# Optimization experiments

Measured on AMD Instinct MI355X. Metric: run time of the kernel, lower is better.

The kernel has to match this reference:

```python
import jax, jax.numpy as jnp
import numpy as np

# Dimensions (see shape_source)
L = 1024   # episode_len (memory slots)
B = 64     # batch (parallel envs)
K = 512    # key_size
V = 512    # value_size
H = 8      # num_head
MEMB = 256 # memory_state_embedding
SDIM = 512 # state_dim
HID = 512  # hidden width of all 2-layer encoders
RIMQ = 512 # rim_query_size
LAT = K - MEMB  # task_inference_latent dim


def setup_inputs() -> dict:
    key = jax.random.key(0)
    ks = jax.random.split(key, 16)
    w = lambda k, shape: (jax.random.normal(k, shape, jnp.float32) * 0.02)
    return {
        "state": jax.random.normal(ks[0], (B, SDIM), jnp.float32),
        "task_inference_latent": jax.random.normal(ks[1], (B, LAT), jnp.float32),
        "keys": jax.random.normal(ks[2], (L, B, K), jnp.float32),
        "vals": jax.random.normal(ks[3], (L, B, V), jnp.float32),
        "rpe_mod": jax.random.uniform(ks[4], (L, B, 1), jnp.float32),
        "step": jnp.maximum(jax.random.randint(ks[5], (B,), 0, L), 1),
        "W_state": w(ks[6], (SDIM, MEMB)), "b_state": jnp.zeros((MEMB,), jnp.float32),
        "Wcq1": w(ks[7], (K, HID)), "bcq1": jnp.zeros((HID,), jnp.float32),
        "Wcq2": w(ks[8], (HID, K)), "bcq2": jnp.zeros((K,), jnp.float32),
        "Wq": w(ks[9], (K, H * K)), "bq": jnp.zeros((H * K,), jnp.float32),
        "Wagg": w(ks[10], (H * V, V)), "bagg": jnp.zeros((V,), jnp.float32),
        "Wrk1": w(ks[11], (V, HID)), "brk1": jnp.zeros((HID,), jnp.float32),
        "Wrk2": w(ks[12], (HID, RIMQ)), "brk2": jnp.zeros((RIMQ,), jnp.float32),
        "Wrv1": w(ks[13], (V, HID)), "brv1": jnp.zeros((HID,), jnp.float32),
        "Wrv2": w(ks[14], (HID, V)), "brv2": jnp.zeros((V,), jnp.float32),
    }


def reference(state, task_inference_latent, keys, vals, rpe_mod, step,
              W_state, b_state, Wcq1, bcq1, Wcq2, bcq2, Wq, bq, Wagg, bagg,
              Wrk1, brk1, Wrk2, brk2, Wrv1, brv1, Wrv2, brv2):
    # DND.read (exploration branch), vectorized over the batch loop.
    se = state @ W_state + b_state                         # state_encoder: [B, MEMB]
    q = jnp.concatenate([se, task_inference_latent], -1)   # [B, K]
    # concat_query_encoder: stacked Linears with NO nonlinearity (faithful to source)
    q = (q @ Wcq1 + bcq1) @ Wcq2 + bcq2                    # [B, K]
    q = (q @ Wq + bq).reshape(B, H, K)                     # multi-head queries

    mk = keys * rpe_mod                                    # RPE-modulated keys [L, B, K]
    scores = jnp.einsum('lbk,bhk->blh', mk, q) / jnp.sqrt(jnp.float32(K))  # [B, L, H]
    valid = jnp.arange(L)[None, :] < step[:, None]         # [B, L] only slots < step[i]
    scores = jnp.where(valid[:, :, None], scores, jnp.float32(-1e30))
    prob = jax.nn.softmax(scores, axis=1) * valid[:, :, None].astype(scores.dtype)

    result = jnp.einsum('blh,lbv->bhv', prob, vals).reshape(B, H * V)
    result = (result @ Wagg + bagg)[:, None, :]            # value_aggregator -> [B, 1, V]
    out_key = (result @ Wrk1 + brk1) @ Wrk2 + brk2         # read_memory_to_key  [B, 1, RIMQ]
    out_val = (result @ Wrv1 + brv1) @ Wrv2 + brv2         # read_memory_to_value [B, 1, V]
    return out_key, out_val
```

## Files before the change

kernel.cpp:

```cpp
#include <hip/hip_runtime.h>
#include <math.h>

#define F4(p)  (*reinterpret_cast<float4*>(p))
#define CF4(p) (*reinterpret_cast<const float4*>(p))

__device__ __forceinline__ void gemm_core(
    const float* __restrict__ Asrc, const float* __restrict__ inbias,
    const float* __restrict__ til,
    int NS, int srcld, int kc, int k0,
    const float* __restrict__ W, int ldw, int n0,
    const float* __restrict__ obias, float* __restrict__ Pout, int ldo)
{
    __shared__ float As[16*64], Ws[16*64];
    const int t = threadIdx.x;
    const int tx = t & 15, ty = t >> 4;
    const int row = t >> 2, kq = (t & 3) * 4;
    const int wrow = t >> 4, wcol = (t & 15) * 4;
    float acc[4][4] = {};
    for (int kk = 0; kk < kc; kk += 16) {
        const int kg = k0 + kk + kq;
        float4 av;
        if (til && kg >= 256) {
            av = CF4(&til[row*256 + (kg - 256)]);
        } else {
            av = {0.f, 0.f, 0.f, 0.f};
            if (inbias) av = CF4(&inbias[kg]);
            for (int s = 0; s < NS; ++s) {
                float4 v = CF4(&Asrc[(size_t)(s*64 + row)*srcld + kg]);
                av.x += v.x; av.y += v.y; av.z += v.z; av.w += v.w;
            }
        }
        As[(kq+0)*64+row] = av.x; As[(kq+1)*64+row] = av.y;
        As[(kq+2)*64+row] = av.z; As[(kq+3)*64+row] = av.w;
        F4(&Ws[wrow*64 + wcol]) = CF4(&W[(size_t)(k0 + kk + wrow)*ldw + n0 + wcol]);
        __syncthreads();
        #pragma unroll
        for (int k = 0; k < 16; ++k) {
            float4 a4 = CF4(&As[k*64 + ty*4]);
            float4 w4 = CF4(&Ws[k*64 + tx*4]);
            float a[4] = {a4.x, a4.y, a4.z, a4.w};
            float w[4] = {w4.x, w4.y, w4.z, w4.w};
            #pragma unroll
            for (int i = 0; i < 4; ++i)
                #pragma unroll
                for (int j = 0; j < 4; ++j)
                    acc[i][j] += a[i] * w[j];
        }
        __syncthreads();
    }
    #pragma unroll
    for (int i = 0; i < 4; ++i) {
        float4 o = {acc[i][0], acc[i][1], acc[i][2], acc[i][3]};
        if (obias) {
            float4 ob = CF4(&obias[n0 + tx*4]);
            o.x += ob.x; o.y += ob.y; o.z += ob.z; o.w += ob.w;
        }
        F4(&Pout[(size_t)(ty*4 + i)*ldo + n0 + tx*4]) = o;
    }
}

__global__ __launch_bounds__(256) void k_q1(
    const float* __restrict__ state, const float* __restrict__ W_state,
    float* __restrict__ P1)
{
    const int nt = blockIdx.x, ks = blockIdx.y;
    gemm_core(state, nullptr, nullptr, 1, 512, 64, ks*64,
              W_state, 256, nt*64, nullptr, P1 + (size_t)ks*64*256, 256);
}

__global__ __launch_bounds__(256) void k_q2(
    const float* __restrict__ P1, const float* __restrict__ b_state,
    const float* __restrict__ til, const float* __restrict__ Wcq1,
    float* __restrict__ P2)
{
    const int nt = blockIdx.x, ks = blockIdx.y;
    gemm_core(P1, b_state, til, 8, 256, 64, ks*64,
              Wcq1, 512, nt*64, nullptr, P2 + (size_t)ks*64*512, 512);
}

__global__ __launch_bounds__(256) void k_q3(
    const float* __restrict__ P2, const float* __restrict__ bcq1,
    const float* __restrict__ Wcq2, float* __restrict__ P3)
{
    const int nt = blockIdx.x, ks = blockIdx.y;
    gemm_core(P2, bcq1, nullptr, 8, 512, 64, ks*64,
              Wcq2, 512, nt*64, nullptr, P3 + (size_t)ks*64*512, 512);
}

__global__ __launch_bounds__(256) void k_qh(
    const float* __restrict__ P3, const float* __restrict__ bcq2,
    const float* __restrict__ Wq, float* __restrict__ P4)
{
    const int nt = blockIdx.x, ks = blockIdx.y;
    gemm_core(P3, bcq2, nullptr, 8, 512, 128, ks*128,
              Wq, 4096, nt*64, nullptr, P4 + (size_t)ks*64*4096, 4096);
}

__global__ __launch_bounds__(256) void k_fa(
    const float* __restrict__ keys, const float* __restrict__ rpe,
    const float* __restrict__ P4, const float* __restrict__ bq,
    const float* __restrict__ vals, const int* __restrict__ step,
    float* __restrict__ Facc, float* __restrict__ Fms)
{
    __shared__ float s_q[4096];
    __shared__ float s_sc[64*8];
    __shared__ float red[256];
    __shared__ float s_m[8];
    const int b = blockIdx.y, lc = blockIdx.x;
    const int sb = step[b];
    const int l0 = lc * 64;
    const int t = threadIdx.x;
    float* facc_out = Facc + ((size_t)(lc*64) + b)*4096;
    if (l0 >= sb) {
        float4 z = {0.f, 0.f, 0.f, 0.f};
        for (int i = t; i < 1024; i += 256) F4(&facc_out[i*4]) = z;
        if (t < 8) {
            size_t o = ((size_t)(lc*64 + b)*8 + t)*2;
            Fms[o] = -1e30f; Fms[o+1] = 0.f;
        }
        return;
    }
    for (int i = t; i < 1024; i += 256) {
        float4 v = CF4(&bq[i*4]);
        #pragma unroll
        for (int s = 0; s < 4; ++s) {
            float4 u = CF4(&P4[(size_t)(s*64 + b)*4096 + i*4]);
            v.x += u.x; v.y += u.y; v.z += u.z; v.w += u.w;
        }
        F4(&s_q[i*4]) = v;
    }
    __syncthreads();
    const int lane = t & 63, w = t >> 6;
    float qr[8][8];
    #pragma unroll
    for (int h = 0; h < 8; ++h) {
        float4 x = CF4(&s_q[h*512 + lane*8]);
        float4 y = CF4(&s_q[h*512 + lane*8 + 4]);
        qr[h][0]=x.x; qr[h][1]=x.y; qr[h][2]=x.z; qr[h][3]=x.w;
        qr[h][4]=y.x; qr[h][5]=y.y; qr[h][6]=y.z; qr[h][7]=y.w;
    }
    const int nl = min(64, sb - l0);
    const float inv_sqrtK = 0.04419417382415922f;
    const bool p0 = lane & 1, p1 = lane & 2, p2 = lane & 4;
    const size_t kstride = (size_t)4*64*512;
    const float* kp = keys + ((size_t)(l0 + w)*64 + b)*512 + lane*8;
    float4 kx, ky;
    if (w < nl) { kx = CF4(kp); ky = CF4(kp + 4); }
    for (int il = w; il < nl; il += 4) {
        float4 nkx, nky;
        if (il + 4 < nl) { nkx = CF4(kp + kstride); nky = CF4(kp + kstride + 4); }
        float kv[8] = {kx.x,kx.y,kx.z,kx.w, ky.x,ky.y,ky.z,ky.w};
        float pr[8] = {};
        #pragma unroll
        for (int h = 0; h < 8; ++h)
            #pragma unroll
            for (int j = 0; j < 8; ++j)
                pr[h] += kv[j] * qr[h][j];
        float w4[4], x2[2], y;
        #pragma unroll
        for (int i = 0; i < 4; ++i) {
            float keep = p0 ? pr[2*i+1] : pr[2*i];
            float send = p0 ? pr[2*i]   : pr[2*i+1];
            w4[i] = keep + __shfl_xor(send, 1);
        }
        #pragma unroll
        for (int i = 0; i < 2; ++i) {
            float keep = p1 ? w4[2*i+1] : w4[2*i];
            float send = p1 ? w4[2*i]   : w4[2*i+1];
            x2[i] = keep + __shfl_xor(send, 2);
        }
        {
            float keep = p2 ? x2[1] : x2[0];
            float send = p2 ? x2[0] : x2[1];
            y = keep + __shfl_xor(send, 4);
        }
        y += __shfl_xor(y, 8);
        y += __shfl_xor(y, 16);
        y += __shfl_xor(y, 32);
        if (lane < 8)
            s_sc[il*8 + lane] = y * rpe[(l0 + il)*64 + b] * inv_sqrtK;
        kx = nkx; ky = nky; kp += kstride;
    }
    __syncthreads();
    const int h = t & 7, g = t >> 3;
    float m = -1e30f;
    for (int l = g; l < nl; l += 32) m = fmaxf(m, s_sc[l*8 + h]);
    red[g*8 + h] = m;
    __syncthreads();
    #pragma unroll
    for (int s = 16; s; s >>= 1) {
        if (g < s) red[g*8+h] = fmaxf(red[g*8+h], red[(g+s)*8+h]);
        __syncthreads();
    }
    if (t < 8) s_m[t] = red[t];
    __syncthreads();
    float mh = s_m[h], s_acc = 0.f;
    for (int l = g; l < nl; l += 32) {
        float e = __expf(s_sc[l*8 + h] - mh);
        s_sc[l*8 + h] = e;
        s_acc += e;
    }
    red[g*8 + h] = s_acc;
    __syncthreads();
    #pragma unroll
    for (int s = 16; s; s >>= 1) {
        if (g < s) red[g*8+h] += red[(g+s)*8+h];
        __syncthreads();
    }
    if (t < 8) {
        size_t o = ((size_t)(lc*64 + b)*8 + t)*2;
        Fms[o] = s_m[t]; Fms[o+1] = red[t];
    }
    const int par = t >> 7, c = t & 127;
    float4 acc[8] = {};
    const size_t vstride = (size_t)2*64*512;
    const float* vp = vals + ((size_t)(l0 + par)*64 + b)*512 + c*4;
    float4 v;
    if (par < nl) v = CF4(vp);
    for (int il = par; il < nl; il += 2) {
        float4 nv;
        if (il + 2 < nl) nv = CF4(vp + vstride);
        float4 pa = CF4(&s_sc[il*8]);
        float4 pb = CF4(&s_sc[il*8 + 4]);
        acc[0].x += pa.x*v.x; acc[0].y += pa.x*v.y; acc[0].z += pa.x*v.z; acc[0].w += pa.x*v.w;
        acc[1].x += pa.y*v.x; acc[1].y += pa.y*v.y; acc[1].z += pa.y*v.z; acc[1].w += pa.y*v.w;
        acc[2].x += pa.z*v.x; acc[2].y += pa.z*v.y; acc[2].z += pa.z*v.z; acc[2].w += pa.z*v.w;
        acc[3].x += pa.w*v.x; acc[3].y += pa.w*v.y; acc[3].z += pa.w*v.z; acc[3].w += pa.w*v.w;
        acc[4].x += pb.x*v.x; acc[4].y += pb.x*v.y; acc[4].z += pb.x*v.z; acc[4].w += pb.x*v.w;
        acc[5].x += pb.y*v.x; acc[5].y += pb.y*v.y; acc[5].z += pb.y*v.z; acc[5].w += pb.y*v.w;
        acc[6].x += pb.z*v.x; acc[6].y += pb.z*v.y; acc[6].z += pb.z*v.z; acc[6].w += pb.z*v.w;
        acc[7].x += pb.w*v.x; acc[7].y += pb.w*v.y; acc[7].z += pb.w*v.z; acc[7].w += pb.w*v.w;
        v = nv; vp += vstride;
    }
    __syncthreads();
    if (par == 1) {
        #pragma unroll
        for (int hh = 0; hh < 8; ++hh)
            F4(&s_q[(c*8 + hh)*4]) = acc[hh];
    }
    __syncthreads();
    if (par == 0) {
        #pragma unroll
        for (int hh = 0; hh < 8; ++hh) {
            float4 o = CF4(&s_q[(c*8 + hh)*4]);
            o.x += acc[hh].x; o.y += acc[hh].y; o.z += acc[hh].z; o.w += acc[hh].w;
            F4(&facc_out[hh*512 + c*4]) = o;
        }
    }
}

__global__ __launch_bounds__(256) void k_comb(
    const float* __restrict__ Facc, const float* __restrict__ Fms,
    float* __restrict__ res)
{
    __shared__ float wgt[16*8];
    const int b = blockIdx.x, t = threadIdx.x;
    if (t < 8) {
        float mm[16], ss[16], e[16];
        float M = -1e30f;
        #pragma unroll
        for (int i = 0; i < 16; ++i) {
            size_t o = ((size_t)(i*64 + b)*8 + t)*2;
            mm[i] = Fms[o]; ss[i] = Fms[o+1];
            M = fmaxf(M, mm[i]);
        }
        float D = 0.f;
        #pragma unroll
        for (int i = 0; i < 16; ++i) { e[i] = __expf(mm[i] - M); D += e[i]*ss[i]; }
        float invD = 1.f / D;
        #pragma unroll
        for (int i = 0; i < 16; ++i) wgt[i*8 + t] = e[i] * invD;
    }
    __syncthreads();
    #pragma unroll
    for (int j = 0; j < 4; ++j) {
        int f = t + j*256;
        int h = f >> 7;
        float4 a = {0.f, 0.f, 0.f, 0.f};
        #pragma unroll
        for (int i = 0; i < 16; ++i) {
            float wi = wgt[i*8 + h];
            float4 v = CF4(&Facc[((size_t)(i*64) + b)*4096 + f*4]);
            a.x += wi*v.x; a.y += wi*v.y; a.z += wi*v.z; a.w += wi*v.w;
        }
        F4(&res[(size_t)b*4096 + f*4]) = a;
    }
}

__global__ __launch_bounds__(256) void k_agg(
    const float* __restrict__ res, const float* __restrict__ Wagg,
    float* __restrict__ P5)
{
    const int nt = blockIdx.x, ks = blockIdx.y;
    gemm_core(res, nullptr, nullptr, 1, 4096, 128, ks*128,
              Wagg, 512, nt*64, nullptr, P5 + (size_t)ks*64*512, 512);
}

__global__ __launch_bounds__(256) void k_rkv1(
    const float* __restrict__ P5, const float* __restrict__ bagg,
    const float* __restrict__ Wrk1, const float* __restrict__ Wrv1,
    float* __restrict__ P6)
{
    const int nt = blockIdx.x, ks = blockIdx.y, z = blockIdx.z;
    gemm_core(P5, bagg, nullptr, 32, 512, 128, ks*128,
              z ? Wrv1 : Wrk1, 512, nt*64,
              nullptr, P6 + (size_t)(z*4 + ks)*64*512, 512);
}

__global__ __launch_bounds__(256) void k_rkv2(
    const float* __restrict__ P6,
    const float* __restrict__ brk1, const float* __restrict__ brv1,
    const float* __restrict__ Wrk2, const float* __restrict__ Wrv2,
    const float* __restrict__ brk2, const float* __restrict__ brv2,
    float* __restrict__ out)
{
    const int nt = blockIdx.x, z = blockIdx.z;
    gemm_core(P6 + (size_t)z*4*64*512, z ? brv1 : brk1, nullptr, 4, 512, 512, 0,
              z ? Wrv2 : Wrk2, 512, nt*64,
              z ? brv2 : brk2, out + (size_t)z*64*512, 512);
}

extern "C" void kernel_launch(void* const* d_in, const int* in_sizes, int n_in,
                              void* d_out, int out_size, void* d_ws, size_t ws_size,
                              hipStream_t stream) {
    const float* state   = (const float*)d_in[0];
    const float* til     = (const float*)d_in[1];
    const float* keys    = (const float*)d_in[2];
    const float* vals    = (const float*)d_in[3];
    const float* rpe     = (const float*)d_in[4];
    const int*   step    = (const int*)d_in[5];
    const float* W_state = (const float*)d_in[6];
    const float* b_state = (const float*)d_in[7];
    const float* Wcq1 = (const float*)d_in[8];
    const float* bcq1 = (const float*)d_in[9];
    const float* Wcq2 = (const float*)d_in[10];
    const float* bcq2 = (const float*)d_in[11];
    const float* Wq   = (const float*)d_in[12];
    const float* bq   = (const float*)d_in[13];
    const float* Wagg = (const float*)d_in[14];
    const float* bagg = (const float*)d_in[15];
    const float* Wrk1 = (const float*)d_in[16];
    const float* brk1 = (const float*)d_in[17];
    const float* Wrk2 = (const float*)d_in[18];
    const float* brk2 = (const float*)d_in[19];
    const float* Wrv1 = (const float*)d_in[20];
    const float* brv1 = (const float*)d_in[21];
    const float* Wrv2 = (const float*)d_in[22];
    const float* brv2 = (const float*)d_in[23];
    float* out = (float*)d_out;
    float* ws  = (float*)d_ws;

    float* P1   = ws;
    float* P2   = ws + 131072;
    float* P3   = ws + 393216;
    float* P4   = ws + 655360;
    float* P5   = ws;
    float* P6   = ws + 1048576;
    float* res  = ws + 1310720;
    float* Facc = ws + 1703936;
    float* Fms  = ws + 5898240;

    k_q1  <<<dim3(4,8),   256, 0, stream>>>(state, W_state, P1);
    k_q2  <<<dim3(8,8),   256, 0, stream>>>(P1, b_state, til, Wcq1, P2);
    k_q3  <<<dim3(8,8),   256, 0, stream>>>(P2, bcq1, Wcq2, P3);
    k_qh  <<<dim3(64,4),  256, 0, stream>>>(P3, bcq2, Wq, P4);
    k_fa  <<<dim3(16,64), 256, 0, stream>>>(keys, rpe, P4, bq, vals, step, Facc, Fms);
    k_comb<<<64, 256, 0, stream>>>(Facc, Fms, res);
    k_agg <<<dim3(8,32),  256, 0, stream>>>(res, Wagg, P5);
    k_rkv1<<<dim3(8,4,2), 256, 0, stream>>>(P5, bagg, Wrk1, Wrv1, P6);
    k_rkv2<<<dim3(8,1,2), 256, 0, stream>>>(P6, brk1, brv1, Wrk2, Wrv2,
                                            brk2, brv2, out);
}
```

Measured before the change: 166.3 us.

## Balance attention chunks across valid slots and deepen key/value prefetch

Each batch row's valid slot range [0, step) is now split evenly across the 16 blocks instead of fixed 64-slot chunks, so no blocks sit idle when step is small and no block gets a full chunk while others get none. The query split-K reduction plus bias is moved into a separate k_qsum kernel, so it is not recomputed in all 16 blocks per batch row. Key and value loads are prefetched two or three iterations ahead instead of one, to hide more memory latency. The cost is an extra kernel launch, a reshuffled workspace layout, and more registers held for prefetched data.

```diff
diff --git a/kernel.cpp b/kernel.cpp
--- a/kernel.cpp
+++ b/kernel.cpp
@@ -96,10 +96,28 @@
               Wq, 4096, nt*64, nullptr, P4 + (size_t)ks*64*4096, 4096);
 }
 
+__global__ __launch_bounds__(256) void k_qsum(
+    const float* __restrict__ P4, const float* __restrict__ bq,
+    float* __restrict__ qh)
+{
+    const int b = blockIdx.x, t = threadIdx.x;
+    #pragma unroll
+    for (int j = 0; j < 4; ++j) {
+        int f = t + j*256;
+        float4 v = CF4(&bq[f*4]);
+        #pragma unroll
+        for (int s = 0; s < 4; ++s) {
+            float4 u = CF4(&P4[(size_t)(s*64 + b)*4096 + f*4]);
+            v.x += u.x; v.y += u.y; v.z += u.z; v.w += u.w;
+        }
+        F4(&qh[(size_t)b*4096 + f*4]) = v;
+    }
+}
+
 __global__ __launch_bounds__(256) void k_fa(
     const float* __restrict__ keys, const float* __restrict__ rpe,
-    const float* __restrict__ P4, const float* __restrict__ bq,
-    const float* __restrict__ vals, const int* __restrict__ step,
+    const float* __restrict__ qh, const float* __restrict__ vals,
+    const int* __restrict__ step,
     float* __restrict__ Facc, float* __restrict__ Fms)
 {
     __shared__ float s_q[4096];
@@ -108,10 +126,12 @@
     __shared__ float s_m[8];
     const int b = blockIdx.y, lc = blockIdx.x;
     const int sb = step[b];
-    const int l0 = lc * 64;
+    const int l0 = (lc * sb) >> 4;
+    const int l1 = ((lc + 1) * sb) >> 4;
+    const int nl = l1 - l0;
     const int t = threadIdx.x;
     float* facc_out = Facc + ((size_t)(lc*64) + b)*4096;
-    if (l0 >= sb) {
+    if (nl <= 0) {
         float4 z = {0.f, 0.f, 0.f, 0.f};
         for (int i = t; i < 1024; i += 256) F4(&facc_out[i*4]) = z;
         if (t < 8) {
@@ -120,15 +140,8 @@
         }
         return;
     }
-    for (int i = t; i < 1024; i += 256) {
-        float4 v = CF4(&bq[i*4]);
-        #pragma unroll
-        for (int s = 0; s < 4; ++s) {
-            float4 u = CF4(&P4[(size_t)(s*64 + b)*4096 + i*4]);
-            v.x += u.x; v.y += u.y; v.z += u.z; v.w += u.w;
-        }
-        F4(&s_q[i*4]) = v;
-    }
+    for (int i = t; i < 1024; i += 256)
+        F4(&s_q[i*4]) = CF4(&qh[(size_t)b*4096 + i*4]);
     __syncthreads();
     const int lane = t & 63, w = t >> 6;
     float qr[8][8];
@@ -139,17 +152,18 @@
         qr[h][0]=x.x; qr[h][1]=x.y; qr[h][2]=x.z; qr[h][3]=x.w;
         qr[h][4]=y.x; qr[h][5]=y.y; qr[h][6]=y.z; qr[h][7]=y.w;
     }
-    const int nl = min(64, sb - l0);
     const float inv_sqrtK = 0.04419417382415922f;
     const bool p0 = lane & 1, p1 = lane & 2, p2 = lane & 4;
     const size_t kstride = (size_t)4*64*512;
     const float* kp = keys + ((size_t)(l0 + w)*64 + b)*512 + lane*8;
-    float4 kx, ky;
-    if (w < nl) { kx = CF4(kp); ky = CF4(kp + 4); }
+    float4 k0x, k0y, k1x, k1y;
+    if (w < nl)     { k0x = CF4(kp);           k0y = CF4(kp + 4); }
+    if (w + 4 < nl) { k1x = CF4(kp + kstride); k1y = CF4(kp + kstride + 4); }
     for (int il = w; il < nl; il += 4) {
-        float4 nkx, nky;
-        if (il + 4 < nl) { nkx = CF4(kp + kstride); nky = CF4(kp + kstride + 4); }
-        float kv[8] = {kx.x,kx.y,kx.z,kx.w, ky.x,ky.y,ky.z,ky.w};
+        float kv[8] = {k0x.x,k0x.y,k0x.z,k0x.w, k0y.x,k0y.y,k0y.z,k0y.w};
+        k0x = k1x; k0y = k1y;
+        if (il + 8 < nl) { k1x = CF4(kp + 2*kstride); k1y = CF4(kp + 2*kstride + 4); }
+        kp += kstride;
         float pr[8] = {};
         #pragma unroll
         for (int h = 0; h < 8; ++h)
@@ -179,7 +193,6 @@
         y += __shfl_xor(y, 32);
         if (lane < 8)
             s_sc[il*8 + lane] = y * rpe[(l0 + il)*64 + b] * inv_sqrtK;
-        kx = nkx; ky = nky; kp += kstride;
     }
     __syncthreads();
     const int h = t & 7, g = t >> 3;
@@ -215,22 +228,24 @@
     float4 acc[8] = {};
     const size_t vstride = (size_t)2*64*512;
     const float* vp = vals + ((size_t)(l0 + par)*64 + b)*512 + c*4;
-    float4 v;
-    if (par < nl) v = CF4(vp);
+    float4 v0, v1, v2;
+    if (par < nl)     v0 = CF4(vp);
+    if (par + 2 < nl) v1 = CF4(vp + vstride);
+    if (par + 4 < nl) v2 = CF4(vp + 2*vstride);
     for (int il = par; il < nl; il += 2) {
-        float4 nv;
-        if (il + 2 < nl) nv = CF4(vp + vstride);
         float4 pa = CF4(&s_sc[il*8]);
         float4 pb = CF4(&s_sc[il*8 + 4]);
-        acc[0].x += pa.x*v.x; acc[0].y += pa.x*v.y; acc[0].z += pa.x*v.z; acc[0].w += pa.x*v.w;
-        acc[1].x += pa.y*v.x; acc[1].y += pa.y*v.y; acc[1].z += pa.y*v.z; acc[1].w += pa.y*v.w;
-        acc[2].x += pa.z*v.x; acc[2].y += pa.z*v.y; acc[2].z += pa.z*v.z; acc[2].w += pa.z*v.w;
-        acc[3].x += pa.w*v.x; acc[3].y += pa.w*v.y; acc[3].z += pa.w*v.z; acc[3].w += pa.w*v.w;
-        acc[4].x += pb.x*v.x; acc[4].y += pb.x*v.y; acc[4].z += pb.x*v.z; acc[4].w += pb.x*v.w;
-        acc[5].x += pb.y*v.x; acc[5].y += pb.y*v.y; acc[5].z += pb.y*v.z; acc[5].w += pb.y*v.w;
-        acc[6].x += pb.z*v.x; acc[6].y += pb.z*v.y; acc[6].z += pb.z*v.z; acc[6].w += pb.z*v.w;
-        acc[7].x += pb.w*v.x; acc[7].y += pb.w*v.y; acc[7].z += pb.w*v.z; acc[7].w += pb.w*v.w;
-        v = nv; vp += vstride;
+        acc[0].x += pa.x*v0.x; acc[0].y += pa.x*v0.y; acc[0].z += pa.x*v0.z; acc[0].w += pa.x*v0.w;
+        acc[1].x += pa.y*v0.x; acc[1].y += pa.y*v0.y; acc[1].z += pa.y*v0.z; acc[1].w += pa.y*v0.w;
+        acc[2].x += pa.z*v0.x; acc[2].y += pa.z*v0.y; acc[2].z += pa.z*v0.z; acc[2].w += pa.z*v0.w;
+        acc[3].x += pa.w*v0.x; acc[3].y += pa.w*v0.y; acc[3].z += pa.w*v0.z; acc[3].w += pa.w*v0.w;
+        acc[4].x += pb.x*v0.x; acc[4].y += pb.x*v0.y; acc[4].z += pb.x*v0.z; acc[4].w += pb.x*v0.w;
+        acc[5].x += pb.y*v0.x; acc[5].y += pb.y*v0.y; acc[5].z += pb.y*v0.z; acc[5].w += pb.y*v0.w;
+        acc[6].x += pb.z*v0.x; acc[6].y += pb.z*v0.y; acc[6].z += pb.z*v0.z; acc[6].w += pb.z*v0.w;
+        acc[7].x += pb.w*v0.x; acc[7].y += pb.w*v0.y; acc[7].z += pb.w*v0.z; acc[7].w += pb.w*v0.w;
+        v0 = v1; v1 = v2;
+        if (il + 6 < nl) v2 = CF4(vp + 3*vstride);
+        vp += vstride;
     }
     __syncthreads();
     if (par == 1) {
@@ -354,17 +369,19 @@
     float* P2   = ws + 131072;
     float* P3   = ws + 393216;
     float* P4   = ws + 655360;
+    float* qh   = ws + 1703936;
+    float* Facc = ws + 1966080;
+    float* Fms  = ws + 6160384;
+    float* res  = ws + 6176768;
     float* P5   = ws;
     float* P6   = ws + 1048576;
-    float* res  = ws + 1310720;
-    float* Facc = ws + 1703936;
-    float* Fms  = ws + 5898240;
 
     k_q1  <<<dim3(4,8),   256, 0, stream>>>(state, W_state, P1);
     k_q2  <<<dim3(8,8),   256, 0, stream>>>(P1, b_state, til, Wcq1, P2);
     k_q3  <<<dim3(8,8),   256, 0, stream>>>(P2, bcq1, Wcq2, P3);
     k_qh  <<<dim3(64,4),  256, 0, stream>>>(P3, bcq2, Wq, P4);
-    k_fa  <<<dim3(16,64), 256, 0, stream>>>(keys, rpe, P4, bq, vals, step, Facc, Fms);
+    k_qsum<<<64, 256, 0, stream>>>(P4, bq, qh);
+    k_fa  <<<dim3(16,64), 256, 0, stream>>>(keys, rpe, qh, vals, step, Facc, Fms);
     k_comb<<<64, 256, 0, stream>>>(Facc, Fms, res);
     k_agg <<<dim3(8,32),  256, 0, stream>>>(res, Wagg, P5);
     k_rkv1<<<dim3(8,4,2), 256, 0, stream>>>(P5, bagg, Wrk1, Wrv1, P6);
```

New measurement: 156.2 us. -6.1%, faster.
